# Optimization experiments

Measured on AMD Instinct MI355X. Metric: run time of the kernel, lower is better.

Reference implementation:

```python
import jax, jax.numpy as jnp
import numpy as np

CHUNK = 64  # output-column tile to bound the [M, K, CHUNK] intermediate


def _mam(A, B):
    """Multiply-and-max/min 'matmul': C[m,n] = max_k(A[m,k]*B[k,n]) + min_k(A[m,k]*B[k,n]).
    A: [M, K], B: [K, N]. Tiled over N to avoid materializing [M, K, N]."""
    M, K = A.shape
    N = B.shape[1]
    assert N % CHUNK == 0
    # [N/CHUNK, K, CHUNK]
    B_tiles = B.reshape(K, N // CHUNK, CHUNK).transpose(1, 0, 2)

    def step(carry, B_blk):
        # prod: [M, K, CHUNK]
        prod = A[:, :, None] * B_blk[None, :, :]
        out = prod.max(axis=1) + prod.min(axis=1)  # [M, CHUNK]
        return carry, out

    _, tiles = jax.lax.scan(step, 0, B_tiles)  # [N/CHUNK, M, CHUNK]
    return tiles.transpose(1, 0, 2).reshape(M, N)


def setup_inputs() -> dict:
    key = jax.random.key(0)
    k1, k2, k3 = jax.random.split(key, 3)
    M, K, N = 2048, 1024, 1024
    x = jax.random.normal(k1, (M, K), dtype=jnp.float32)
    # torch stores weight as [out_features, in_features]
    weight = jax.random.normal(k2, (N, K), dtype=jnp.float32) * (1.0 / np.sqrt(K))
    bias = jax.random.normal(k3, (N,), dtype=jnp.float32) * (1.0 / np.sqrt(K))
    return {"x": x, "weight": weight, "bias": bias}


def reference(x, weight, bias):
    # beta == 0 (beta=False): forward is MAM(x, W^T) + bias
    C = _mam(x, weight.T)
    return C + bias[None, :]
```

## Files before the change

kernel.cpp:

```cpp
#include <hip/hip_runtime.h>
#include <math.h>


#define TS 64
#define BK 16
#define RSF 156
#define STRIPF (8 * RSF)

typedef __attribute__((ext_vector_type(2))) float f32x2;
typedef __attribute__((ext_vector_type(4))) float f32x4;

__device__ __forceinline__ f32x2 lo2(f32x4 v) { return __builtin_shufflevector(v, v, 0, 1); }
__device__ __forceinline__ f32x2 hi2(f32x4 v) { return __builtin_shufflevector(v, v, 2, 3); }

__device__ __forceinline__ void mam_upd_pk(float& mx, float& mn, f32x2 a, f32x2 b) {
    f32x2 p = a * b;
    asm("v_max3_f32 %0, %1, %2, %0" : "+v"(mx) : "v"(p.x), "v"(p.y));
    asm("v_min3_f32 %0, %1, %2, %0" : "+v"(mn) : "v"(p.x), "v"(p.y));
}

__global__
__attribute__((amdgpu_flat_work_group_size(256, 256)))
__attribute__((amdgpu_waves_per_eu(2, 2)))
void mam_sk(
    const float* __restrict__ A, const float* __restrict__ W,
    const float* __restrict__ bias, float* __restrict__ C,
    int M, int N, int K)
{
    __shared__ __align__(16) float smem[8 * STRIPF];
    float* cmx = smem;
    float* cmn = smem + TS * TS;

    const int t    = threadIdx.x;
    const int w    = t >> 6;
    const int lane = t & 63;
    const int ty   = lane >> 3;
    const int tx   = lane & 7;
    const int m0   = blockIdx.y * TS;
    const int n0   = blockIdx.x * TS;
    const int kc   = K >> 2;
    const int kb0  = w * kc;

    const int sr = lane >> 2;
    const int sc = lane & 3;

    float* sAw = smem + (size_t)w * STRIPF;
    float* sWw = smem + (size_t)(4 + w) * STRIPF;

    const float* Ap = A + (size_t)(m0 + sr) * K + kb0 + sc * 4;
    const float* Wp = W + (size_t)(n0 + sr) * K + kb0 + sc * 4;

    float mx[8][8], mn[8][8];
#pragma unroll
    for (int i = 0; i < 8; ++i)
#pragma unroll
        for (int j = 0; j < 8; ++j) {
            mx[i][j] = -INFINITY;
            mn[i][j] =  INFINITY;
        }

    float4 ra[4], rw[4];
#pragma unroll
    for (int q = 0; q < 4; ++q) {
        ra[q] = *(const float4*)(Ap + (size_t)q * 16 * K);
        rw[q] = *(const float4*)(Wp + (size_t)q * 16 * K);
    }
    Ap += BK;
    Wp += BK;

    const int mo = 20 * (sr >> 3) + 2 * (sr & 7);

    const int nStages = kc / BK;
    for (int s = 0; s < nStages; ++s) {
#pragma unroll
        for (int q = 0; q < 4; ++q) {
            const int po = mo + 40 * q;
            *(float2*)&sAw[(sc * 2 + 0) * RSF + po] = make_float2(ra[q].x, ra[q].y);
            *(float2*)&sAw[(sc * 2 + 1) * RSF + po] = make_float2(ra[q].z, ra[q].w);
            *(float2*)&sWw[(sc * 2 + 0) * RSF + po] = make_float2(rw[q].x, rw[q].y);
            *(float2*)&sWw[(sc * 2 + 1) * RSF + po] = make_float2(rw[q].z, rw[q].w);
        }
        if (s + 1 < nStages) {
#pragma unroll
            for (int q = 0; q < 4; ++q) {
                ra[q] = *(const float4*)(Ap + (size_t)q * 16 * K);
                rw[q] = *(const float4*)(Wp + (size_t)q * 16 * K);
            }
            Ap += BK;
            Wp += BK;
        }

#pragma unroll
        for (int kp = 0; kp < BK / 2; ++kp) {
            const float* rA = sAw + kp * RSF + ty * 20;
            const float* rW = sWw + kp * RSF + tx * 20;
            f32x4 A0 = *(const f32x4*)(rA + 0);
            f32x4 A1 = *(const f32x4*)(rA + 4);
            f32x4 A2 = *(const f32x4*)(rA + 8);
            f32x4 A3 = *(const f32x4*)(rA + 12);
            f32x4 W0 = *(const f32x4*)(rW + 0);
            f32x4 W1 = *(const f32x4*)(rW + 4);
            f32x4 W2 = *(const f32x4*)(rW + 8);
            f32x4 W3 = *(const f32x4*)(rW + 12);

            f32x2 av[8] = {lo2(A0), hi2(A0), lo2(A1), hi2(A1),
                           lo2(A2), hi2(A2), lo2(A3), hi2(A3)};
            f32x2 bv[8] = {lo2(W0), hi2(W0), lo2(W1), hi2(W1),
                           lo2(W2), hi2(W2), lo2(W3), hi2(W3)};

#pragma unroll
            for (int i = 0; i < 8; ++i)
#pragma unroll
                for (int j = 0; j < 8; ++j)
                    mam_upd_pk(mx[i][j], mn[i][j], av[i], bv[j]);
        }
    }

    __syncthreads();

    for (int rnd = 0; rnd < 4; ++rnd) {
        if (w == rnd) {
#pragma unroll
            for (int i = 0; i < 8; ++i)
#pragma unroll
                for (int j = 0; j < 8; ++j) {
                    const int idx = (ty * 8 + i) * TS + tx * 8 + j;
                    if (rnd == 0) {
                        cmx[idx] = mx[i][j];
                        cmn[idx] = mn[i][j];
                    } else {
                        cmx[idx] = fmaxf(cmx[idx], mx[i][j]);
                        cmn[idx] = fminf(cmn[idx], mn[i][j]);
                    }
                }
        }
        __syncthreads();
    }

    float4 blo = *(const float4*)(bias + n0 + tx * 8);
    float4 bhi = *(const float4*)(bias + n0 + tx * 8 + 4);
#pragma unroll
    for (int i2 = 0; i2 < 2; ++i2) {
        const int i   = w * 2 + i2;
        const int row = ty * 8 + i;
        const int idx = row * TS + tx * 8;
        float4 o0, o1;
        o0.x = cmx[idx + 0] + cmn[idx + 0] + blo.x;
        o0.y = cmx[idx + 1] + cmn[idx + 1] + blo.y;
        o0.z = cmx[idx + 2] + cmn[idx + 2] + blo.z;
        o0.w = cmx[idx + 3] + cmn[idx + 3] + blo.w;
        o1.x = cmx[idx + 4] + cmn[idx + 4] + bhi.x;
        o1.y = cmx[idx + 5] + cmn[idx + 5] + bhi.y;
        o1.z = cmx[idx + 6] + cmn[idx + 6] + bhi.z;
        o1.w = cmx[idx + 7] + cmn[idx + 7] + bhi.w;
        float4* p = (float4*)(C + (size_t)(m0 + row) * N + n0 + tx * 8);
        p[0] = o0;
        p[1] = o1;
    }
}

#define BM 64
#define BN 64
#define FBK 32
#define LDSW 68

__device__ __forceinline__ void mam_upd_fb(float& mx, float& mn, float p0, float p1) {
    float nmx, nmn;
    asm("v_max3_f32 %0, %1, %2, %3" : "=v"(nmx) : "v"(p0), "v"(p1), "v"(mx));
    asm("v_min3_f32 %0, %1, %2, %3" : "=v"(nmn) : "v"(p0), "v"(p1), "v"(mn));
    mx = nmx;
    mn = nmn;
}

__global__ __launch_bounds__(256) void mam_fallback(
    const float* __restrict__ A, const float* __restrict__ W,
    const float* __restrict__ bias, float* __restrict__ C,
    int M, int N, int K)
{
    __shared__ float Asf[FBK][LDSW];
    __shared__ float Wsf[FBK][LDSW];

    const int t  = threadIdx.x;
    const int tx = t & 15;
    const int ty = t >> 4;
    const int m0 = blockIdx.y * BM;
    const int n0 = blockIdx.x * BN;
    const int r  = t >> 3;
    const int kq = t & 7;

    const float* Aptr = A + (size_t)(m0 + r) * K + kq * 4;
    const float* Wptr = W + (size_t)(n0 + r) * K + kq * 4;

    float vmax[4][4], vmin[4][4];
#pragma unroll
    for (int i = 0; i < 4; ++i)
#pragma unroll
        for (int j = 0; j < 4; ++j) {
            vmax[i][j] = -INFINITY;
            vmin[i][j] =  INFINITY;
        }

    for (int k0 = 0; k0 < K; k0 += FBK) {
        float4 a0 = *(const float4*)(Aptr);
        float4 a1 = *(const float4*)(Aptr + (size_t)32 * K);
        float4 w0 = *(const float4*)(Wptr);
        float4 w1 = *(const float4*)(Wptr + (size_t)32 * K);
        Aptr += FBK;
        Wptr += FBK;

        const int kk = kq * 4;
        Asf[kk + 0][r]      = a0.x;
        Asf[kk + 1][r]      = a0.y;
        Asf[kk + 2][r]      = a0.z;
        Asf[kk + 3][r]      = a0.w;
        Asf[kk + 0][r + 32] = a1.x;
        Asf[kk + 1][r + 32] = a1.y;
        Asf[kk + 2][r + 32] = a1.z;
        Asf[kk + 3][r + 32] = a1.w;

        Wsf[kk + 0][r]      = w0.x;
        Wsf[kk + 1][r]      = w0.y;
        Wsf[kk + 2][r]      = w0.z;
        Wsf[kk + 3][r]      = w0.w;
        Wsf[kk + 0][r + 32] = w1.x;
        Wsf[kk + 1][r + 32] = w1.y;
        Wsf[kk + 2][r + 32] = w1.z;
        Wsf[kk + 3][r + 32] = w1.w;

        __syncthreads();

#pragma unroll
        for (int k = 0; k < FBK; k += 2) {
            float4 ta0 = *(const float4*)&Asf[k    ][ty * 4];
            float4 ta1 = *(const float4*)&Asf[k + 1][ty * 4];
            float4 tb0 = *(const float4*)&Wsf[k    ][tx * 4];
            float4 tb1 = *(const float4*)&Wsf[k + 1][tx * 4];

            float a0v[4] = {ta0.x, ta0.y, ta0.z, ta0.w};
            float a1v[4] = {ta1.x, ta1.y, ta1.z, ta1.w};
            float b0v[4] = {tb0.x, tb0.y, tb0.z, tb0.w};
            float b1v[4] = {tb1.x, tb1.y, tb1.z, tb1.w};

#pragma unroll
            for (int i = 0; i < 4; ++i)
#pragma unroll
                for (int j = 0; j < 4; ++j) {
                    float p0 = a0v[i] * b0v[j];
                    float p1 = a1v[i] * b1v[j];
                    mam_upd_fb(vmax[i][j], vmin[i][j], p0, p1);
                }
        }
        __syncthreads();
    }

    float4 bv = *(const float4*)(bias + n0 + tx * 4);
#pragma unroll
    for (int i = 0; i < 4; ++i) {
        float4 o;
        o.x = vmax[i][0] + vmin[i][0] + bv.x;
        o.y = vmax[i][1] + vmin[i][1] + bv.y;
        o.z = vmax[i][2] + vmin[i][2] + bv.z;
        o.w = vmax[i][3] + vmin[i][3] + bv.w;
        *(float4*)(C + (size_t)(m0 + ty * 4 + i) * N + n0 + tx * 4) = o;
    }
}

extern "C" void kernel_launch(void* const* d_in, const int* in_sizes, int n_in,
                              void* d_out, int out_size, void* d_ws, size_t ws_size,
                              hipStream_t stream) {
    const float* x    = (const float*)d_in[0];
    const float* w    = (const float*)d_in[1];
    const float* bias = (const float*)d_in[2];
    float* out = (float*)d_out;

    const int N = in_sizes[2];
    const int K = in_sizes[1] / N;
    const int M = in_sizes[0] / K;

    const bool fast_ok = (K % (4 * BK) == 0) && (M % TS == 0) && (N % TS == 0);

    if (fast_ok) {
        dim3 grid(N / TS, M / TS);
        mam_sk<<<grid, 256, 0, stream>>>(x, w, bias, out, M, N, K);
    } else {
        dim3 grid(N / BN, M / BM);
        mam_fallback<<<grid, 256, 0, stream>>>(x, w, bias, out, M, N, K);
    }
}
```

Measured before the change: 170.9 us.

## Shrink N tile to 32, drop packed multiply and register prefetch for occupancy

Halves the output tile width per block (64x32), so each thread holds an 8x4 max/min accumulator instead of 8x8 and the grid doubles. The packed f32x2 multiply is replaced with scalar multiplies, and the global-to-register prefetch for the next stage is removed in favour of load-then-store each stage. The waves-per-EU hint rises from 2 to 3-4 so more waves can hide latency. The trade-off is half the arithmetic per LDS load, more redundant A traffic across blocks, and no software pipelining of global loads.

```diff
diff --git a/kernel.cpp b/kernel.cpp
--- a/kernel.cpp
+++ b/kernel.cpp
@@ -2,117 +2,114 @@
 #include <math.h>
 
 
-#define TS 64
+#define TSM 64
+#define TSN 32
 #define BK 16
-#define RSF 156
-#define STRIPF (8 * RSF)
-
-typedef __attribute__((ext_vector_type(2))) float f32x2;
+#define ARS 156
+#define WRS 92
+#define ASTRIP (8 * ARS)
+#define WSTRIP (8 * WRS)
+#define WAVEF (ASTRIP + WSTRIP)
+
 typedef __attribute__((ext_vector_type(4))) float f32x4;
 
-__device__ __forceinline__ f32x2 lo2(f32x4 v) { return __builtin_shufflevector(v, v, 0, 1); }
-__device__ __forceinline__ f32x2 hi2(f32x4 v) { return __builtin_shufflevector(v, v, 2, 3); }
-
-__device__ __forceinline__ void mam_upd_pk(float& mx, float& mn, f32x2 a, f32x2 b) {
-    f32x2 p = a * b;
-    asm("v_max3_f32 %0, %1, %2, %0" : "+v"(mx) : "v"(p.x), "v"(p.y));
-    asm("v_min3_f32 %0, %1, %2, %0" : "+v"(mn) : "v"(p.x), "v"(p.y));
+__device__ __forceinline__ void mam_upd(float& mx, float& mn, float p0, float p1) {
+    asm("v_max3_f32 %0, %1, %2, %0" : "+v"(mx) : "v"(p0), "v"(p1));
+    asm("v_min3_f32 %0, %1, %2, %0" : "+v"(mn) : "v"(p0), "v"(p1));
 }
 
 __global__
 __attribute__((amdgpu_flat_work_group_size(256, 256)))
-__attribute__((amdgpu_waves_per_eu(2, 2)))
+__attribute__((amdgpu_waves_per_eu(3, 4)))
 void mam_sk(
     const float* __restrict__ A, const float* __restrict__ W,
     const float* __restrict__ bias, float* __restrict__ C,
     int M, int N, int K)
 {
-    __shared__ __align__(16) float smem[8 * STRIPF];
+    __shared__ __align__(16) float smem[4 * WAVEF];
     float* cmx = smem;
-    float* cmn = smem + TS * TS;
+    float* cmn = smem + TSM * TSN;
 
     const int t    = threadIdx.x;
     const int w    = t >> 6;
     const int lane = t & 63;
     const int ty   = lane >> 3;
     const int tx   = lane & 7;
-    const int m0   = blockIdx.y * TS;
-    const int n0   = blockIdx.x * TS;
+    const int m0   = blockIdx.y * TSM;
+    const int n0   = blockIdx.x * TSN;
     const int kc   = K >> 2;
     const int kb0  = w * kc;
 
     const int sr = lane >> 2;
     const int sc = lane & 3;
 
-    float* sAw = smem + (size_t)w * STRIPF;
-    float* sWw = smem + (size_t)(4 + w) * STRIPF;
+    float* sAw = smem + w * WAVEF;
+    float* sWw = sAw + ASTRIP;
 
     const float* Ap = A + (size_t)(m0 + sr) * K + kb0 + sc * 4;
     const float* Wp = W + (size_t)(n0 + sr) * K + kb0 + sc * 4;
 
-    float mx[8][8], mn[8][8];
+    float mx[8][4], mn[8][4];
 #pragma unroll
     for (int i = 0; i < 8; ++i)
 #pragma unroll
-        for (int j = 0; j < 8; ++j) {
+        for (int j = 0; j < 4; ++j) {
             mx[i][j] = -INFINITY;
             mn[i][j] =  INFINITY;
         }
 
-    float4 ra[4], rw[4];
-#pragma unroll
-    for (int q = 0; q < 4; ++q) {
-        ra[q] = *(const float4*)(Ap + (size_t)q * 16 * K);
-        rw[q] = *(const float4*)(Wp + (size_t)q * 16 * K);
-    }
-    Ap += BK;
-    Wp += BK;
-
-    const int mo = 20 * (sr >> 3) + 2 * (sr & 7);
+    const int moA = 20 * (sr >> 3) + 2 * (sr & 7);
+    const int moW = 12 * (sr >> 2) + 2 * (sr & 3);
 
     const int nStages = kc / BK;
     for (int s = 0; s < nStages; ++s) {
+        float4 ra[4], rw[2];
+#pragma unroll
+        for (int q = 0; q < 4; ++q)
+            ra[q] = *(const float4*)(Ap + (size_t)q * 16 * K);
+#pragma unroll
+        for (int q = 0; q < 2; ++q)
+            rw[q] = *(const float4*)(Wp + (size_t)q * 16 * K);
+        Ap += BK;
+        Wp += BK;
+
 #pragma unroll
         for (int q = 0; q < 4; ++q) {
-            const int po = mo + 40 * q;
-            *(float2*)&sAw[(sc * 2 + 0) * RSF + po] = make_float2(ra[q].x, ra[q].y);
-            *(float2*)&sAw[(sc * 2 + 1) * RSF + po] = make_float2(ra[q].z, ra[q].w);
-            *(float2*)&sWw[(sc * 2 + 0) * RSF + po] = make_float2(rw[q].x, rw[q].y);
-            *(float2*)&sWw[(sc * 2 + 1) * RSF + po] = make_float2(rw[q].z, rw[q].w);
-        }
-        if (s + 1 < nStages) {
-#pragma unroll
-            for (int q = 0; q < 4; ++q) {
-                ra[q] = *(const float4*)(Ap + (size_t)q * 16 * K);
-                rw[q] = *(const float4*)(Wp + (size_t)q * 16 * K);
-            }
-            Ap += BK;
-            Wp += BK;
+            const int po = moA + 40 * q;
+            *(float2*)&sAw[(sc * 2 + 0) * ARS + po] = make_float2(ra[q].x, ra[q].y);
+            *(float2*)&sAw[(sc * 2 + 1) * ARS + po] = make_float2(ra[q].z, ra[q].w);
+        }
+#pragma unroll
+        for (int q = 0; q < 2; ++q) {
+            const int po = moW + 48 * q;
+            *(float2*)&sWw[(sc * 2 + 0) * WRS + po] = make_float2(rw[q].x, rw[q].y);
+            *(float2*)&sWw[(sc * 2 + 1) * WRS + po] = make_float2(rw[q].z, rw[q].w);
         }
 
 #pragma unroll
         for (int kp = 0; kp < BK / 2; ++kp) {
-            const float* rA = sAw + kp * RSF + ty * 20;
-            const float* rW = sWw + kp * RSF + tx * 20;
+            const float* rA = sAw + kp * ARS + ty * 20;
+            const float* rW = sWw + kp * WRS + tx * 12;
             f32x4 A0 = *(const f32x4*)(rA + 0);
             f32x4 A1 = *(const f32x4*)(rA + 4);
             f32x4 A2 = *(const f32x4*)(rA + 8);
             f32x4 A3 = *(const f32x4*)(rA + 12);
             f32x4 W0 = *(const f32x4*)(rW + 0);
             f32x4 W1 = *(const f32x4*)(rW + 4);
-            f32x4 W2 = *(const f32x4*)(rW + 8);
-            f32x4 W3 = *(const f32x4*)(rW + 12);
-
-            f32x2 av[8] = {lo2(A0), hi2(A0), lo2(A1), hi2(A1),
-                           lo2(A2), hi2(A2), lo2(A3), hi2(A3)};
-            f32x2 bv[8] = {lo2(W0), hi2(W0), lo2(W1), hi2(W1),
-                           lo2(W2), hi2(W2), lo2(W3), hi2(W3)};
+
+            float a0[8] = {A0.x, A0.z, A1.x, A1.z, A2.x, A2.z, A3.x, A3.z};
+            float a1[8] = {A0.y, A0.w, A1.y, A1.w, A2.y, A2.w, A3.y, A3.w};
+            float b0[4] = {W0.x, W0.z, W1.x, W1.z};
+            float b1[4] = {W0.y, W0.w, W1.y, W1.w};
 
 #pragma unroll
             for (int i = 0; i < 8; ++i)
 #pragma unroll
-                for (int j = 0; j < 8; ++j)
-                    mam_upd_pk(mx[i][j], mn[i][j], av[i], bv[j]);
+                for (int j = 0; j < 4; ++j) {
+                    float p0 = a0[i] * b0[j];
+                    float p1 = a1[i] * b1[j];
+                    mam_upd(mx[i][j], mn[i][j], p0, p1);
+                }
         }
     }
 
@@ -123,8 +120,8 @@
 #pragma unroll
             for (int i = 0; i < 8; ++i)
 #pragma unroll
-                for (int j = 0; j < 8; ++j) {
-                    const int idx = (ty * 8 + i) * TS + tx * 8 + j;
+                for (int j = 0; j < 4; ++j) {
+                    const int idx = (ty * 8 + i) * TSN + tx * 4 + j;
                     if (rnd == 0) {
                         cmx[idx] = mx[i][j];
                         cmn[idx] = mn[i][j];
@@ -137,13 +134,13 @@
         __syncthreads();
     }
 
-    float4 blo = *(const float4*)(bias + n0 + tx * 8);
-    float4 bhi = *(const float4*)(bias + n0 + tx * 8 + 4);
-#pragma unroll
-    for (int i2 = 0; i2 < 2; ++i2) {
-        const int i   = w * 2 + i2;
-        const int row = ty * 8 + i;
-        const int idx = row * TS + tx * 8;
+    {
+        const int row = t >> 2;
+        const int cq  = t & 3;
+        const int col = cq * 8;
+        float4 blo = *(const float4*)(bias + n0 + col);
+        float4 bhi = *(const float4*)(bias + n0 + col + 4);
+        const int idx = row * TSN + col;
         float4 o0, o1;
         o0.x = cmx[idx + 0] + cmn[idx + 0] + blo.x;
         o0.y = cmx[idx + 1] + cmn[idx + 1] + blo.y;
@@ -153,7 +150,7 @@
         o1.y = cmx[idx + 5] + cmn[idx + 5] + bhi.y;
         o1.z = cmx[idx + 6] + cmn[idx + 6] + bhi.z;
         o1.w = cmx[idx + 7] + cmn[idx + 7] + bhi.w;
-        float4* p = (float4*)(C + (size_t)(m0 + row) * N + n0 + tx * 8);
+        float4* p = (float4*)(C + (size_t)(m0 + row) * N + n0 + col);
         p[0] = o0;
         p[1] = o1;
     }
@@ -277,10 +274,10 @@
     const int K = in_sizes[1] / N;
     const int M = in_sizes[0] / K;
 
-    const bool fast_ok = (K % (4 * BK) == 0) && (M % TS == 0) && (N % TS == 0);
+    const bool fast_ok = (K % (4 * BK) == 0) && (M % TSM == 0) && (N % TSN == 0);
 
     if (fast_ok) {
-        dim3 grid(N / TS, M / TS);
+        dim3 grid(N / TSN, M / TSM);
         mam_sk<<<grid, 256, 0, stream>>>(x, w, bias, out, M, N, K);
     } else {
         dim3 grid(N / BN, M / BM);
```

Result: faster. 158.4 us (-7.3%).
